# Performance work log

Measured on AMD Instinct MI355X. Metric: run time of the kernel, lower is better.

## Reference

```python
import jax, jax.numpy as jnp
import numpy as np

SINKHORN_ALPHA = 20.0
WEIGHT_LOSS_ECR = 100.0
OT_MAX_ITER = 100
STOP_THR = 0.005
EPS = 1e-16


def setup_inputs() -> dict:
    key = jax.random.key(0)
    # cost matrix: topics x vocab, nonnegative
    M = jax.random.uniform(key, (2000, 20000), dtype=jnp.float32)
    return {"M": M}


def reference(M):
    n, m = M.shape
    a = jnp.full((n, 1), 1.0 / n, dtype=M.dtype)  # uniform row marginal
    b = jnp.full((m, 1), 1.0 / m, dtype=M.dtype)  # uniform col marginal
    K = jnp.exp(-M * SINKHORN_ALPHA)              # Gibbs kernel, (n, m)

    u0 = jnp.full((n, 1), 1.0 / n, dtype=M.dtype)
    v0 = jnp.zeros((m, 1), dtype=M.dtype)
    err0 = jnp.asarray(1.0, dtype=M.dtype)
    cpt0 = jnp.asarray(0, dtype=jnp.int32)

    def cond(carry):
        u, v, err, cpt = carry
        return (err > STOP_THR) & (cpt < OT_MAX_ITER)

    def body(carry):
        u, v, err, cpt = carry
        v = b / (K.T @ u + EPS)          # (m, 1)
        u = a / (K @ v + EPS)            # (n, 1)
        cpt = cpt + 1
        # convergence check every 50 iterations (cpt % 50 == 1), as in torch
        bb = v * (K.T @ u)               # (m, 1) implied col marginal
        err_new = jnp.max(jnp.sum(jnp.abs(bb - b), axis=0))
        err = jnp.where(cpt % 50 == 1, err_new.astype(err.dtype), err)
        return (u, v, err, cpt)

    u, v, err, cpt = jax.lax.while_loop(cond, body, (u0, v0, err0, cpt0))

    transp = u * (K * v.T)               # transport plan, (n, m)
    loss_ECR = jnp.sum(transp * M)
    return loss_ECR * WEIGHT_LOSS_ECR
```

## Files before the change

### kernel.cpp

```cpp
#include <hip/hip_runtime.h>

typedef unsigned int uint32;
typedef unsigned long long uint64;
typedef float floatx2 __attribute__((ext_vector_type(2)));

#define ROWS_R 2000
#define COLS_R 20000
#define NBLK   256
#define NTHR   1024
#define NWAVE  16
#define CPB    80
#define CSTR   501
#define KDW    (CPB*CSTR)
#define KGUARD 16

static constexpr float A_MARG = 1.0f / 2000.0f;
static constexpr float B_MARG = 1.0f / 20000.0f;
static constexpr float EPSV   = 1e-16f;
static constexpr float THR    = 0.005f;
static constexpr float NALPHA = -20.0f;

__device__ __forceinline__ void st_dev_f32(float* p, float v) {
    __hip_atomic_store(p, v, __ATOMIC_RELAXED, __HIP_MEMORY_SCOPE_AGENT);
}
__device__ __forceinline__ float ld_dev_f32(const float* p) {
    return __hip_atomic_load(const_cast<float*>(p), __ATOMIC_RELAXED, __HIP_MEMORY_SCOPE_AGENT);
}
__device__ __forceinline__ void st_dev_f32x2(float* p, float x, float y) {
    union { float2 f; uint64 q; } u; u.f = make_float2(x, y);
    __hip_atomic_store(reinterpret_cast<uint64*>(p), u.q, __ATOMIC_RELAXED, __HIP_MEMORY_SCOPE_AGENT);
}
__device__ __forceinline__ float2 ld_dev_f32x2(const float* p) {
    union { float2 f; uint64 q; } u;
    u.q = __hip_atomic_load(reinterpret_cast<uint64*>(const_cast<float*>(p)),
                            __ATOMIC_RELAXED, __HIP_MEMORY_SCOPE_AGENT);
    return u.f;
}

__device__ __forceinline__ float halfpair_sum(float x) {
#if __has_builtin(__builtin_amdgcn_permlane32_swap)
    int xi = __float_as_int(x);
    auto sw = __builtin_amdgcn_permlane32_swap(xi, xi, false, false);
    return __int_as_float(sw[0]) + __int_as_float(sw[1]);
#else
    return x + __shfl_xor(x, 32, 64);
#endif
}

__device__ __forceinline__ void grid_barrier(uint32* ctrl, uint32 rnd) {
    asm volatile("s_waitcnt vmcnt(0)" ::: "memory");
    __syncthreads();
    if (threadIdx.x == 0) {
        const int gid = (int)(blockIdx.x >> 5);
        uint32* gcnt = ctrl + 128 + gid * 64;
        uint32* ggen = ctrl + 768 + gid * 64;
        uint32 a = __hip_atomic_fetch_add(gcnt, 1u, __ATOMIC_RELAXED, __HIP_MEMORY_SCOPE_AGENT);
        if (a == rnd * 32u + 31u) {
            uint32 r = __hip_atomic_fetch_add(ctrl, 1u, __ATOMIC_RELAXED, __HIP_MEMORY_SCOPE_AGENT);
            if (r == rnd * 8u + 7u) {
#pragma unroll
                for (int g = 0; g < 8; ++g)
                    __hip_atomic_store(ctrl + 768 + g * 64, rnd + 1u,
                                       __ATOMIC_RELAXED, __HIP_MEMORY_SCOPE_AGENT);
            }
        }
        while (__hip_atomic_load(ggen, __ATOMIC_RELAXED, __HIP_MEMORY_SCOPE_AGENT) < rnd + 1u)
            __builtin_amdgcn_s_sleep(1);
    }
    __syncthreads();
}

__global__ __launch_bounds__(256) void init_kernel(float* __restrict__ u_g,
                                                   uint32* __restrict__ ctrl,
                                                   float* __restrict__ err2,
                                                   float* __restrict__ loss) {
    int idx = blockIdx.x * 256 + threadIdx.x;
    if (idx < 1280) ctrl[idx] = 0u;
    if (idx == 0) { err2[0] = 0.f; err2[1] = 0.f; *loss = 0.f; }
    if (idx < 2048) u_g[idx] = (idx < ROWS_R) ? A_MARG : 0.0f;
}

__global__ __launch_bounds__(NTHR, 1) void sinkhorn_lds(
    const float* __restrict__ M,
    float* __restrict__ u_g,
    float* __restrict__ P,
    uint32* __restrict__ ctrl,
    float* __restrict__ err2,
    float* __restrict__ loss,
    float* __restrict__ out) {
    __shared__ uint32 sK[KDW + KGUARD];
    __shared__ float  s_vloc[CPB];
    __shared__ float  s_vprev[CPB];
    __shared__ float  s_red[NWAVE * 8];
    __shared__ int    s_flag;

    const int tid  = threadIdx.x;
    const int lane = tid & 63;
    const int wav  = tid >> 6;
    const int b    = blockIdx.x;
    const int j0   = b * CPB;
    uint32 bar = 0;

    for (int i = tid; i < KDW + KGUARD; i += NTHR) sK[i] = 0u;
    __syncthreads();
    for (int q = wav; q < 500; q += NWAVE) {
#pragma unroll
        for (int ph = 0; ph < 2; ++ph) {
            const int cl = ph * 64 + lane;
            const int j  = j0 + cl;
            if ((ph == 0 || lane < 16) && j < COLS_R) {
                const float* mp = M + (size_t)(4 * q) * COLS_R + j;
                float k0 = __expf(NALPHA * mp[0]);
                float k1 = __expf(NALPHA * mp[COLS_R]);
                float k2 = __expf(NALPHA * mp[2 * COLS_R]);
                float k3 = __expf(NALPHA * mp[3 * COLS_R]);
                int lo = __builtin_amdgcn_cvt_pk_fp8_f32(k0, k1, 0, false);
                int hi = __builtin_amdgcn_cvt_pk_fp8_f32(k2, k3, lo, true);
                sK[cl * CSTR + q] = (uint32)hi;
            }
        }
    }
    __syncthreads();

    for (int t = 1; t <= 100; ++t) {
        const bool chk  = (t == 2) || (t == 52);
        const int  slot = (t == 52) ? 1 : 0;

        float4 u_r[8];
#pragma unroll
        for (int s = 0; s < 8; ++s) {
            const float* up = u_g + (size_t)(s * 64 + lane) * 4;
            float2 a0 = ld_dev_f32x2(up);
            float2 a1 = ld_dev_f32x2(up + 2);
            u_r[s] = make_float4(a0.x, a0.y, a1.x, a1.y);
        }

        float e = 0.f;
#pragma unroll
        for (int q = 0; q < 5; ++q) {
            const int jl = wav * 5 + q;
            float acc = 0.f;
#pragma unroll
            for (int s = 0; s < 8; ++s) {
                uint32 kw = sK[jl * CSTR + s * 64 + lane];
                floatx2 f01 = __builtin_amdgcn_cvt_pk_f32_fp8(kw, false);
                floatx2 f23 = __builtin_amdgcn_cvt_pk_f32_fp8(kw, true);
                acc += f01.x * u_r[s].x + f01.y * u_r[s].y + f23.x * u_r[s].z + f23.y * u_r[s].w;
            }
            acc = halfpair_sum(acc);
#pragma unroll
            for (int o = 16; o; o >>= 1) acc += __shfl_xor(acc, o, 64);
            if (lane == 0) {
                float vnew = B_MARG / (acc + EPSV);
                if (chk) {
                    float vold = s_vloc[jl];
                    s_vprev[jl] = vold;
                    if (j0 + jl < COLS_R) e += fabsf(vold * acc - B_MARG);
                }
                s_vloc[jl] = vnew;
            }
        }
        if (chk && lane == 0) s_red[wav] = e;
        __syncthreads();

        float4 pa = make_float4(0.f, 0.f, 0.f, 0.f);
#pragma unroll 8
        for (int jp = 0; jp < 40; ++jp) {
            const int cl = 2 * jp + (lane >> 5);
            const int m  = lane & 31;
            uint32 kw = sK[cl * CSTR + wav * 32 + m];
            float  vv = s_vloc[cl];
            floatx2 f01 = __builtin_amdgcn_cvt_pk_f32_fp8(kw, false);
            floatx2 f23 = __builtin_amdgcn_cvt_pk_f32_fp8(kw, true);
            pa.x += f01.x * vv; pa.y += f01.y * vv;
            pa.z += f23.x * vv; pa.w += f23.y * vv;
        }
        pa.x = halfpair_sum(pa.x);
        pa.y = halfpair_sum(pa.y);
        pa.z = halfpair_sum(pa.z);
        pa.w = halfpair_sum(pa.w);
        if (lane < 32) {
            float* dst = P + (size_t)b * 2048 + wav * 128 + 4 * lane;
            st_dev_f32x2(dst,     pa.x, pa.y);
            st_dev_f32x2(dst + 2, pa.z, pa.w);
        }

        if (chk && tid == 0) {
            float s = 0.f;
            for (int k = 0; k < NWAVE; ++k) s += s_red[k];
            if (s != 0.f) atomicAdd(&err2[slot], s);
        }
        grid_barrier(ctrl, bar++);

        if (chk) {
            if (tid == 0) s_flag = (ld_dev_f32(&err2[slot]) <= THR) ? 1 : 0;
            __syncthreads();
            if (s_flag) {
                if (tid < CPB) s_vloc[tid] = s_vprev[tid];
                __syncthreads();
                break;
            }
        }

        {
            float v0 = ld_dev_f32(P + (size_t)(tid >> 3) * 2048 + 8 * b + (tid & 7));
            float v1 = ld_dev_f32(P + (size_t)((tid >> 3) + 128) * 2048 + 8 * b + (tid & 7));
            float s = v0 + v1;
            s += __shfl_xor(s, 8, 64);
            s += __shfl_xor(s, 16, 64);
            s = halfpair_sum(s);
            if (lane < 8) s_red[wav * 8 + lane] = s;
        }
        __syncthreads();
        if (tid < 8) {
            float s = 0.f;
            for (int w = 0; w < NWAVE; ++w) s += s_red[w * 8 + tid];
            const int row = 8 * b + tid;
            float val = (row < ROWS_R) ? A_MARG / (s + EPSV) : 0.0f;
            st_dev_f32(&u_g[row], val);
        }
        grid_barrier(ctrl, bar++);
    }

    {
        float acc = 0.f;
        for (int r = wav; r < ROWS_R; r += NWAVE) {
            const float uu = ld_dev_f32(&u_g[r]);
            const float* mp = M + (size_t)r * COLS_R + j0;
#pragma unroll
            for (int ph = 0; ph < 2; ++ph) {
                const int cl = ph * 64 + lane;
                if ((ph == 0 || lane < 16) && (j0 + cl) < COLS_R) {
                    float m = mp[cl];
                    acc += uu * __expf(NALPHA * m) * s_vloc[cl] * m;
                }
            }
        }
        acc = halfpair_sum(acc);
#pragma unroll
        for (int o = 16; o; o >>= 1) acc += __shfl_xor(acc, o, 64);
        if (lane == 0) s_red[wav] = acc;
        __syncthreads();
        if (tid == 0) {
            float s = 0.f;
            for (int k = 0; k < NWAVE; ++k) s += s_red[k];
            if (s != 0.f) atomicAdd(loss, s);
        }
    }
    grid_barrier(ctrl, bar++);
    if (b == 0 && tid == 0) out[0] = ld_dev_f32(loss) * 100.0f;
}


__device__ __forceinline__ float block_reduce_sum256(float v) {
#pragma unroll
    for (int o = 32; o; o >>= 1) v += __shfl_down(v, o, 64);
    __shared__ float smem[4];
    int lane = threadIdx.x & 63, w = threadIdx.x >> 6;
    if (lane == 0) smem[w] = v;
    __syncthreads();
    v = (threadIdx.x < 4) ? smem[threadIdx.x] : 0.0f;
    v += __shfl_down(v, 2, 64);
    v += __shfl_down(v, 1, 64);
    return v;
}

__global__ __launch_bounds__(256) void fb_init(float* u, float* vden, int* done, float* err, float* loss) {
    int idx = blockIdx.x * 256 + threadIdx.x;
    if (idx == 0) { *done = 0; *err = 0.0f; *loss = 0.0f; }
    if (idx < ROWS_R) u[idx] = A_MARG;
    if (idx < COLS_R) vden[idx] = 0.0f;
}
__global__ __launch_bounds__(256) void fb_colpass(const float* __restrict__ M, const float* __restrict__ u,
                                                  float* __restrict__ vden, const int* __restrict__ done) {
    if (*done) return;
    int c4 = blockIdx.x * 256 + threadIdx.x;
    if (c4 >= 5000) return;
    int r0 = blockIdx.y * 50;
    float4 acc = make_float4(0.f, 0.f, 0.f, 0.f);
    for (int r = r0; r < r0 + 50; ++r) {
        float ui = u[r];
        float4 mm = reinterpret_cast<const float4*>(M)[(size_t)r * 5000 + c4];
        acc.x += __expf(NALPHA * mm.x) * ui; acc.y += __expf(NALPHA * mm.y) * ui;
        acc.z += __expf(NALPHA * mm.z) * ui; acc.w += __expf(NALPHA * mm.w) * ui;
    }
    atomicAdd(&vden[c4 * 4 + 0], acc.x); atomicAdd(&vden[c4 * 4 + 1], acc.y);
    atomicAdd(&vden[c4 * 4 + 2], acc.z); atomicAdd(&vden[c4 * 4 + 3], acc.w);
}
__global__ __launch_bounds__(256) void fb_finv(float* v, float* vden, const int* done) {
    if (*done) return;
    int j = blockIdx.x * 256 + threadIdx.x;
    if (j < COLS_R) { v[j] = B_MARG / (vden[j] + EPSV); vden[j] = 0.0f; }
}
__global__ __launch_bounds__(256) void fb_rowpass(const float* __restrict__ M, const float* __restrict__ v,
                                                  float* __restrict__ u, const int* __restrict__ done) {
    if (*done) return;
    int row = blockIdx.x;
    const float4* v4 = reinterpret_cast<const float4*>(v);
    float acc = 0.0f;
    for (int c4 = threadIdx.x; c4 < 5000; c4 += 256) {
        float4 mm = reinterpret_cast<const float4*>(M)[(size_t)row * 5000 + c4];
        float4 vv = v4[c4];
        acc += __expf(NALPHA * mm.x) * vv.x + __expf(NALPHA * mm.y) * vv.y
             + __expf(NALPHA * mm.z) * vv.z + __expf(NALPHA * mm.w) * vv.w;
    }
    float s = block_reduce_sum256(acc);
    if (threadIdx.x == 0) u[row] = A_MARG / (s + EPSV);
}
__global__ __launch_bounds__(256) void fb_errfin(const float* v, float* vden, float* err, const int* done) {
    if (*done) return;
    int j = blockIdx.x * 256 + threadIdx.x;
    float local = 0.0f;
    if (j < COLS_R) { local = fabsf(v[j] * vden[j] - B_MARG); vden[j] = 0.0f; }
    float s = block_reduce_sum256(local);
    if (threadIdx.x == 0) atomicAdd(err, s);
}
__global__ void fb_check(int* done, float* err) {
    if (threadIdx.x == 0) { if (!*done && *err <= THR) *done = 1; *err = 0.0f; }
}
__global__ __launch_bounds__(256) void fb_loss(const float* __restrict__ M, const float* __restrict__ u,
                                               const float* __restrict__ v, float* __restrict__ loss) {
    int row = blockIdx.x;
    const float4* M4p = reinterpret_cast<const float4*>(M + (size_t)row * COLS_R);
    const float4* v4 = reinterpret_cast<const float4*>(v);
    float acc = 0.0f;
    for (int c4 = threadIdx.x; c4 < 5000; c4 += 256) {
        float4 mm = M4p[c4]; float4 vv = v4[c4];
        acc += __expf(NALPHA * mm.x) * vv.x * mm.x + __expf(NALPHA * mm.y) * vv.y * mm.y
             + __expf(NALPHA * mm.z) * vv.z * mm.z + __expf(NALPHA * mm.w) * vv.w * mm.w;
    }
    float s = block_reduce_sum256(acc);
    if (threadIdx.x == 0) atomicAdd(loss, s * u[row]);
}
__global__ void fb_writeout(float* out, const float* loss) {
    if (threadIdx.x == 0) out[0] = *loss * 100.0f;
}


extern "C" void kernel_launch(void* const* d_in, const int* in_sizes, int n_in,
                              void* d_out, int out_size, void* d_ws, size_t ws_size,
                              hipStream_t stream) {
    const float* M = (const float*)d_in[0];
    char* base = (char*)d_ws;

    const size_t OFF_CTRL = 0;
    const size_t OFF_ERR  = 8192;
    const size_t OFF_LOSS = 8320;
    const size_t OFF_U    = 8448;
    const size_t OFF_P    = OFF_U + 8192 + 256;
    const size_t NEED     = OFF_P + (size_t)NBLK * 2048 * 4;

    if (ws_size >= NEED) {
        uint32* ctrl = (uint32*)(base + OFF_CTRL);
        float*  err2 = (float*)(base + OFF_ERR);
        float*  loss = (float*)(base + OFF_LOSS);
        float*  u_g  = (float*)(base + OFF_U);
        float*  P    = (float*)(base + OFF_P);

        init_kernel<<<8, 256, 0, stream>>>(u_g, ctrl, err2, loss);
        sinkhorn_lds<<<NBLK, NTHR, 0, stream>>>(M, u_g, P, ctrl, err2, loss, (float*)d_out);
    } else {
        int*   done = (int*)(base + 0);
        float* err  = (float*)(base + 8);
        float* loss = (float*)(base + 16);
        float* u    = (float*)(base + 64);
        float* v    = (float*)(base + 64 + 8192);
        float* vden = (float*)(base + 64 + 8192 + 80000);

        fb_init<<<79, 256, 0, stream>>>(u, vden, done, err, loss);
        dim3 cgrid(20, 40);
        for (int t = 1; t <= 100; ++t) {
            fb_colpass<<<cgrid, 256, 0, stream>>>(M, u, vden, done);
            fb_finv<<<79, 256, 0, stream>>>(v, vden, done);
            fb_rowpass<<<ROWS_R, 256, 0, stream>>>(M, v, u, done);
            if (t == 1 || t == 51) {
                fb_colpass<<<cgrid, 256, 0, stream>>>(M, u, vden, done);
                fb_errfin<<<79, 256, 0, stream>>>(v, vden, err, done);
                fb_check<<<1, 64, 0, stream>>>(done, err);
            }
        }
        fb_loss<<<ROWS_R, 256, 0, stream>>>(M, u, v, loss);
        fb_writeout<<<1, 64, 0, stream>>>((float*)d_out, loss);
    }
}
```

Before: 354.5 us.

## Replace grid barriers with per-block flag polling and double-buffered u

Removes the two hierarchical atomic grid barriers per Sinkhorn iteration. Each block now publishes a per-block progress flag after writing its partials and after writing its slice of u, and consumers poll only the flags they need. The u vector is double-buffered by iteration parity so the next column pass can start without a full barrier. The convergence check and final loss reduction use arrival counters instead of barriers. This trades one global rendezvous for 256-way flag polling by 256 threads per block, and it relies on careful memory ordering under relaxed atomics.

Result: slower. 361.9 us (+2.1%).

```diff
diff --git a/kernel.cpp b/kernel.cpp
--- a/kernel.cpp
+++ b/kernel.cpp
@@ -26,6 +26,12 @@
 __device__ __forceinline__ float ld_dev_f32(const float* p) {
     return __hip_atomic_load(const_cast<float*>(p), __ATOMIC_RELAXED, __HIP_MEMORY_SCOPE_AGENT);
 }
+__device__ __forceinline__ void st_dev_u32(uint32* p, uint32 v) {
+    __hip_atomic_store(p, v, __ATOMIC_RELAXED, __HIP_MEMORY_SCOPE_AGENT);
+}
+__device__ __forceinline__ uint32 ld_dev_u32(const uint32* p) {
+    return __hip_atomic_load(const_cast<uint32*>(p), __ATOMIC_RELAXED, __HIP_MEMORY_SCOPE_AGENT);
+}
 __device__ __forceinline__ void st_dev_f32x2(float* p, float x, float y) {
     union { float2 f; uint64 q; } u; u.f = make_float2(x, y);
     __hip_atomic_store(reinterpret_cast<uint64*>(p), u.q, __ATOMIC_RELAXED, __HIP_MEMORY_SCOPE_AGENT);
@@ -47,46 +53,23 @@
 #endif
 }
 
-__device__ __forceinline__ void grid_barrier(uint32* ctrl, uint32 rnd) {
-    asm volatile("s_waitcnt vmcnt(0)" ::: "memory");
-    __syncthreads();
-    if (threadIdx.x == 0) {
-        const int gid = (int)(blockIdx.x >> 5);
-        uint32* gcnt = ctrl + 128 + gid * 64;
-        uint32* ggen = ctrl + 768 + gid * 64;
-        uint32 a = __hip_atomic_fetch_add(gcnt, 1u, __ATOMIC_RELAXED, __HIP_MEMORY_SCOPE_AGENT);
-        if (a == rnd * 32u + 31u) {
-            uint32 r = __hip_atomic_fetch_add(ctrl, 1u, __ATOMIC_RELAXED, __HIP_MEMORY_SCOPE_AGENT);
-            if (r == rnd * 8u + 7u) {
-#pragma unroll
-                for (int g = 0; g < 8; ++g)
-                    __hip_atomic_store(ctrl + 768 + g * 64, rnd + 1u,
-                                       __ATOMIC_RELAXED, __HIP_MEMORY_SCOPE_AGENT);
-            }
-        }
-        while (__hip_atomic_load(ggen, __ATOMIC_RELAXED, __HIP_MEMORY_SCOPE_AGENT) < rnd + 1u)
-            __builtin_amdgcn_s_sleep(1);
-    }
-    __syncthreads();
-}
-
-__global__ __launch_bounds__(256) void init_kernel(float* __restrict__ u_g,
-                                                   uint32* __restrict__ ctrl,
-                                                   float* __restrict__ err2,
-                                                   float* __restrict__ loss) {
+__global__ __launch_bounds__(256) void init_kernel(float* __restrict__ ubuf,
+                                                   uint32* __restrict__ flags,
+                                                   float* __restrict__ fm,
+                                                   uint32* __restrict__ um) {
     int idx = blockIdx.x * 256 + threadIdx.x;
-    if (idx < 1280) ctrl[idx] = 0u;
-    if (idx == 0) { err2[0] = 0.f; err2[1] = 0.f; *loss = 0.f; }
-    if (idx < 2048) u_g[idx] = (idx < ROWS_R) ? A_MARG : 0.0f;
+    if (idx < 2048) flags[idx] = 0u;
+    if (idx == 0) { fm[0] = 0.f; fm[1] = 0.f; fm[2] = 0.f; um[0] = 0u; um[1] = 0u; um[2] = 0u; }
+    if (idx < 2048) ubuf[idx] = (idx < ROWS_R) ? A_MARG : 0.0f;
 }
 
 __global__ __launch_bounds__(NTHR, 1) void sinkhorn_lds(
     const float* __restrict__ M,
-    float* __restrict__ u_g,
+    float* __restrict__ ubuf,
     float* __restrict__ P,
-    uint32* __restrict__ ctrl,
-    float* __restrict__ err2,
-    float* __restrict__ loss,
+    uint32* __restrict__ flags,
+    float* __restrict__ fm,
+    uint32* __restrict__ um,
     float* __restrict__ out) {
     __shared__ uint32 sK[KDW + KGUARD];
     __shared__ float  s_vloc[CPB];
@@ -99,7 +82,8 @@
     const int wav  = tid >> 6;
     const int b    = blockIdx.x;
     const int j0   = b * CPB;
-    uint32 bar = 0;
+    uint32* pflag = flags;
+    uint32* uflag = flags + 1024;
 
     for (int i = tid; i < KDW + KGUARD; i += NTHR) sK[i] = 0u;
     __syncthreads();
@@ -122,14 +106,26 @@
     }
     __syncthreads();
 
+    int ubsel = 0;
+    int broke = 0;
+
     for (int t = 1; t <= 100; ++t) {
         const bool chk  = (t == 2) || (t == 52);
         const int  slot = (t == 52) ? 1 : 0;
 
+        if (t > 1) {
+            if (tid < 256) {
+                uint32* f = &uflag[tid * 4];
+                while (ld_dev_u32(f) < (uint32)(t - 1)) __builtin_amdgcn_s_sleep(1);
+            }
+        }
+        __syncthreads();
+
+        const float* ub = ubuf + (size_t)((t - 1) & 1) * 2048;
         float4 u_r[8];
 #pragma unroll
         for (int s = 0; s < 8; ++s) {
-            const float* up = u_g + (size_t)(s * 64 + lane) * 4;
+            const float* up = ub + (size_t)(s * 64 + lane) * 4;
             float2 a0 = ld_dev_f32x2(up);
             float2 a1 = ld_dev_f32x2(up + 2);
             u_r[s] = make_float4(a0.x, a0.y, a1.x, a1.y);
@@ -185,23 +181,39 @@
             st_dev_f32x2(dst + 2, pa.z, pa.w);
         }
 
-        if (chk && tid == 0) {
-            float s = 0.f;
-            for (int k = 0; k < NWAVE; ++k) s += s_red[k];
-            if (s != 0.f) atomicAdd(&err2[slot], s);
-        }
-        grid_barrier(ctrl, bar++);
+        asm volatile("s_waitcnt vmcnt(0)" ::: "memory");
+        __syncthreads();
+        if (tid == 0) {
+            st_dev_u32(&pflag[b * 4], (uint32)t);
+            if (chk) {
+                float s = 0.f;
+                for (int k = 0; k < NWAVE; ++k) s += s_red[k];
+                if (s != 0.f) atomicAdd(&fm[slot], s);
+                asm volatile("s_waitcnt vmcnt(0)" ::: "memory");
+                __hip_atomic_fetch_add(&um[slot], 1u, __ATOMIC_RELAXED, __HIP_MEMORY_SCOPE_AGENT);
+            }
+        }
 
         if (chk) {
-            if (tid == 0) s_flag = (ld_dev_f32(&err2[slot]) <= THR) ? 1 : 0;
+            if (tid == 0) {
+                while (ld_dev_u32(&um[slot]) < (uint32)NBLK) __builtin_amdgcn_s_sleep(1);
+                s_flag = (ld_dev_f32(&fm[slot]) <= THR) ? 1 : 0;
+            }
             __syncthreads();
             if (s_flag) {
                 if (tid < CPB) s_vloc[tid] = s_vprev[tid];
                 __syncthreads();
+                ubsel = (t - 1) & 1;
+                broke = 1;
                 break;
             }
         }
 
+        if (tid < 256) {
+            uint32* f = &pflag[tid * 4];
+            while (ld_dev_u32(f) < (uint32)t) __builtin_amdgcn_s_sleep(1);
+        }
+        __syncthreads();
         {
             float v0 = ld_dev_f32(P + (size_t)(tid >> 3) * 2048 + 8 * b + (tid & 7));
             float v1 = ld_dev_f32(P + (size_t)((tid >> 3) + 128) * 2048 + 8 * b + (tid & 7));
@@ -217,15 +229,28 @@
             for (int w = 0; w < NWAVE; ++w) s += s_red[w * 8 + tid];
             const int row = 8 * b + tid;
             float val = (row < ROWS_R) ? A_MARG / (s + EPSV) : 0.0f;
-            st_dev_f32(&u_g[row], val);
-        }
-        grid_barrier(ctrl, bar++);
-    }
+            st_dev_f32(ubuf + (size_t)(t & 1) * 2048 + row, val);
+        }
+        if (wav == 0) {
+            asm volatile("s_waitcnt vmcnt(0)" ::: "memory");
+            if (lane == 0) st_dev_u32(&uflag[b * 4], (uint32)t);
+        }
+        ubsel = t & 1;
+    }
+
+    if (!broke) {
+        if (tid < 256) {
+            uint32* f = &uflag[tid * 4];
+            while (ld_dev_u32(f) < 100u) __builtin_amdgcn_s_sleep(1);
+        }
+    }
+    __syncthreads();
 
     {
+        const float* uf = ubuf + (size_t)ubsel * 2048;
         float acc = 0.f;
         for (int r = wav; r < ROWS_R; r += NWAVE) {
-            const float uu = ld_dev_f32(&u_g[r]);
+            const float uu = ld_dev_f32(uf + r);
             const float* mp = M + (size_t)r * COLS_R + j0;
 #pragma unroll
             for (int ph = 0; ph < 2; ++ph) {
@@ -244,11 +269,15 @@
         if (tid == 0) {
             float s = 0.f;
             for (int k = 0; k < NWAVE; ++k) s += s_red[k];
-            if (s != 0.f) atomicAdd(loss, s);
-        }
-    }
-    grid_barrier(ctrl, bar++);
-    if (b == 0 && tid == 0) out[0] = ld_dev_f32(loss) * 100.0f;
+            if (s != 0.f) atomicAdd(&fm[2], s);
+            asm volatile("s_waitcnt vmcnt(0)" ::: "memory");
+            __hip_atomic_fetch_add(&um[2], 1u, __ATOMIC_RELAXED, __HIP_MEMORY_SCOPE_AGENT);
+        }
+    }
+    if (b == 0 && tid == 0) {
+        while (ld_dev_u32(&um[2]) < (uint32)NBLK) __builtin_amdgcn_s_sleep(1);
+        out[0] = ld_dev_f32(&fm[2]) * 100.0f;
+    }
 }
 
 
@@ -343,22 +372,22 @@
     const float* M = (const float*)d_in[0];
     char* base = (char*)d_ws;
 
-    const size_t OFF_CTRL = 0;
-    const size_t OFF_ERR  = 8192;
-    const size_t OFF_LOSS = 8320;
-    const size_t OFF_U    = 8448;
-    const size_t OFF_P    = OFF_U + 8192 + 256;
-    const size_t NEED     = OFF_P + (size_t)NBLK * 2048 * 4;
+    const size_t OFF_FLAGS = 0;
+    const size_t OFF_FM    = 8192;
+    const size_t OFF_UM    = 8192 + 128;
+    const size_t OFF_U     = 8448;
+    const size_t OFF_P     = OFF_U + 16384;
+    const size_t NEED      = OFF_P + (size_t)NBLK * 2048 * 4;
 
     if (ws_size >= NEED) {
-        uint32* ctrl = (uint32*)(base + OFF_CTRL);
-        float*  err2 = (float*)(base + OFF_ERR);
-        float*  loss = (float*)(base + OFF_LOSS);
-        float*  u_g  = (float*)(base + OFF_U);
-        float*  P    = (float*)(base + OFF_P);
-
-        init_kernel<<<8, 256, 0, stream>>>(u_g, ctrl, err2, loss);
-        sinkhorn_lds<<<NBLK, NTHR, 0, stream>>>(M, u_g, P, ctrl, err2, loss, (float*)d_out);
+        uint32* flags = (uint32*)(base + OFF_FLAGS);
+        float*  fm    = (float*)(base + OFF_FM);
+        uint32* um    = (uint32*)(base + OFF_UM);
+        float*  ubuf  = (float*)(base + OFF_U);
+        float*  P     = (float*)(base + OFF_P);
+
+        init_kernel<<<8, 256, 0, stream>>>(ubuf, flags, fm, um);
+        sinkhorn_lds<<<NBLK, NTHR, 0, stream>>>(M, ubuf, P, flags, fm, um, (float*)d_out);
     } else {
         int*   done = (int*)(base + 0);
         float* err  = (float*)(base + 8);
```
